# Kernel tuning notes

Hardware: AMD Instinct MI355X
Metric: run time of the kernel (lower is better)

## Reference

```python
import jax, jax.numpy as jnp
import numpy as np

N_NODES = 60000
N_EDGES = 120000
N_GRAPHS = 2048
ATOM_DIM = 4
H = 192            # hidden_dim
NL = 5             # n_layers
ND = 200           # n_descriptors
EDGE_DIM = 1


def setup_inputs() -> dict:
    key = jax.random.key(0)
    ks = jax.random.split(key, 16)

    def w(k, shape, fan_in):
        return jax.random.normal(k, shape, jnp.float32) * (1.0 / np.sqrt(fan_in))

    M_IN = 2 * H + EDGE_DIM  # message MLP input: [x_src, x_dst, edge_attr]
    M_H = 2 * H              # MPNNLayer(hidden_dim=hidden_dim*2)
    inp = {
        "atom_features": jax.random.normal(ks[0], (N_NODES, ATOM_DIM), jnp.float32),
        "edge_attr": jax.random.normal(ks[1], (N_EDGES, EDGE_DIM), jnp.float32),
        "edge_index": jax.random.randint(ks[2], (2, N_EDGES), 0, N_NODES),
        "batch": jnp.sort(jax.random.randint(ks[3], (N_NODES,), 0, N_GRAPHS)),
        # atom encoder: Linear + GELU + LayerNorm
        "enc_w": w(ks[4], (ATOM_DIM, H), ATOM_DIM), "enc_b": jnp.zeros((H,), jnp.float32),
        "enc_ln_g": jnp.ones((H,), jnp.float32), "enc_ln_b": jnp.zeros((H,), jnp.float32),
        # 5 MPNN layers (stacked params)
        "msg_w1": w(ks[5], (NL, M_IN, M_H), M_IN), "msg_b1": jnp.zeros((NL, M_H), jnp.float32),
        "msg_w2": w(ks[6], (NL, M_H, H), M_H), "msg_b2": jnp.zeros((NL, H), jnp.float32),
        "upd_w": w(ks[7], (NL, 2 * H, H), 2 * H), "upd_b": jnp.zeros((NL, H), jnp.float32),
        "ln_g": jnp.ones((NL, H), jnp.float32), "ln_b": jnp.zeros((NL, H), jnp.float32),
        # head MLP: 2H -> H -> H//2 -> ND
        "h1_w": w(ks[8], (2 * H, H), 2 * H), "h1_b": jnp.zeros((H,), jnp.float32),
        "h2_w": w(ks[9], (H, H // 2), H), "h2_b": jnp.zeros((H // 2,), jnp.float32),
        "h3_w": w(ks[10], (H // 2, ND), H // 2), "h3_b": jnp.zeros((ND,), jnp.float32),
    }
    return inp


def _ln(x, g, b, eps=1e-5):
    mu = x.mean(-1, keepdims=True)
    v = x.var(-1, keepdims=True)
    return (x - mu) / jnp.sqrt(v + eps) * g + b


def _gelu(x):
    return jax.nn.gelu(x, approximate=False)  # torch nn.GELU (erf)


def _forward(atom_features, edge_attr, enc_w, enc_b, enc_ln_g, enc_ln_b,
             msg_w1, msg_b1, msg_w2, msg_b2, upd_w, upd_b, ln_g, ln_b,
             h1_w, h1_b, h2_w, h2_b, h3_w, h3_b, edge_index, batch):
    src, dst = edge_index[0], edge_index[1]
    x = _ln(_gelu(atom_features @ enc_w + enc_b), enc_ln_g, enc_ln_b)  # [N, H]
    for l in range(NL):
        # gather endpoints -> message MLP -> scatter-sum to dst
        m_in = jnp.concatenate([x[src], x[dst], edge_attr], axis=-1)   # [E, 2H+1]
        m = _gelu(m_in @ msg_w1[l] + msg_b1[l]) @ msg_w2[l] + msg_b2[l]  # [E, H]
        agg = jax.ops.segment_sum(m, dst, num_segments=N_NODES)        # [N, H]
        x_new = _gelu(jnp.concatenate([x, agg], axis=-1) @ upd_w[l] + upd_b[l])
        x = _ln(x + x_new, ln_g[l], ln_b[l])  # residual + LN (dropout = eval identity)
    # per-graph mean/max pooling (segment reductions)
    cnt = jax.ops.segment_sum(jnp.ones((x.shape[0],), x.dtype), batch, num_segments=N_GRAPHS)
    s = jax.ops.segment_sum(x, batch, num_segments=N_GRAPHS)
    mean_pool = jnp.where(cnt[:, None] > 0, s / jnp.maximum(cnt, 1.0)[:, None], 0.0)
    max_pool = jax.ops.segment_max(x, batch, num_segments=N_GRAPHS)  # -inf for empty, as torch
    g = jnp.concatenate([mean_pool, max_pool], axis=-1)  # [G, 2H]
    h = _gelu(g @ h1_w + h1_b)
    h = _gelu(h @ h2_w + h2_b)
    return h @ h3_w + h3_b  # [G, ND]


def reference(atom_features, edge_attr, edge_index, batch, enc_w, enc_b, enc_ln_g, enc_ln_b,
              msg_w1, msg_b1, msg_w2, msg_b2, upd_w, upd_b, ln_g, ln_b,
              h1_w, h1_b, h2_w, h2_b, h3_w, h3_b):
    return _forward(atom_features, edge_attr, enc_w, enc_b, enc_ln_g, enc_ln_b,
                    msg_w1, msg_b1, msg_w2, msg_b2, upd_w, upd_b, ln_g, ln_b,
                    h1_w, h1_b, h2_w, h2_b, h3_w, h3_b, edge_index, batch)
```

## Files before the change

kernel.cpp:

```cpp
#include <hip/hip_runtime.h>

#define H 192
#define NL 5
#define NN 60000
#define NE 120000
#define NG 2048
#define ND 200
#define LDA 392
#define NT 128
#define LDU 200

typedef __bf16 bfrag __attribute__((ext_vector_type(8)));
typedef __bf16 bf16x4 __attribute__((ext_vector_type(4)));
typedef float f32x4 __attribute__((ext_vector_type(4)));

__device__ __forceinline__ unsigned short f2bf(float f) {
  union { float f; unsigned u; } v; v.f = f;
  return (unsigned short)((v.u + 0x7FFFu + ((v.u >> 16) & 1u)) >> 16);
}
__device__ __forceinline__ float bflo(unsigned u) {
  union { unsigned u; float f; } v; v.u = u << 16; return v.f;
}
__device__ __forceinline__ float bfhi(unsigned u) {
  union { unsigned u; float f; } v; v.u = u & 0xffff0000u; return v.f;
}
__device__ __forceinline__ float gelu(float x) {
  const float t = exp2f(x * (-2.3020922f - 0.10293942f * x * x));
  return x * __frcp_rn(1.f + t);
}

__global__ __launch_bounds__(256) void prep_kernel(
    const float* __restrict__ msg_w1, const float* __restrict__ msg_w2,
    const float* __restrict__ upd_w, const float* __restrict__ h1_w,
    const float* __restrict__ h2_w, const float* __restrict__ h3_w,
    unsigned short* __restrict__ W1f, float* __restrict__ w1last,
    unsigned short* __restrict__ W2f, unsigned short* __restrict__ Uf,
    float* __restrict__ h1t, float* __restrict__ h2t, float* __restrict__ h3t) {
  int idx = blockIdx.x * 256 + threadIdx.x;
  const int SW1 = NL * 147456;
  const int S2 = NL * 384;
  const int SW2 = NL * 73728;
  if (idx < SW1) {
    int l = idx / 147456, r = idx % 147456;
    int i = r & 7, lane = (r >> 3) & 63, t = r >> 9;
    int kk = t % 12, jblk = t / 12;
    int j = jblk * 16 + (lane & 15);
    int k = kk * 32 + ((lane >> 4) << 3) + i;
    W1f[idx] = f2bf(msg_w1[(size_t)l * 385 * 384 + (size_t)k * 384 + j]);
    return;
  }
  idx -= SW1;
  if (idx < S2) {
    int l = idx / 384, j = idx % 384;
    w1last[idx] = msg_w1[(size_t)l * 385 * 384 + 384 * 384 + j];
    return;
  }
  idx -= S2;
  if (idx < SW2) {
    int l = idx / 73728, r = idx % 73728;
    int i = r & 7, lane = (r >> 3) & 63, t = r >> 9;
    int kk = t % 12, jblk = t / 12;
    int j = jblk * 16 + (lane & 15);
    int k = kk * 32 + ((lane >> 4) << 3) + i;
    W2f[idx] = f2bf(msg_w2[(size_t)l * 384 * 192 + (size_t)k * 192 + j]);
    return;
  }
  idx -= SW2;
  if (idx < SW2) {
    int l = idx / 73728, r = idx % 73728;
    int i = r & 7, lane = (r >> 3) & 63, t = r >> 9;
    int kk = t % 12, jblk = t / 12;
    int j = jblk * 16 + (lane & 15);
    int k = kk * 32 + ((lane >> 4) << 3) + i;
    Uf[idx] = f2bf(upd_w[(size_t)l * 384 * 192 + (size_t)k * 192 + j]);
    return;
  }
  idx -= SW2;
  if (idx < 192 * 384) { int j = idx / 384, k = idx % 384; h1t[idx] = h1_w[k * 192 + j]; return; }
  idx -= 192 * 384;
  if (idx < 96 * 192) { int j = idx / 192, k = idx % 192; h2t[idx] = h2_w[k * 96 + j]; return; }
  idx -= 96 * 192;
  if (idx < 200 * 96) { int j = idx / 96, k = idx % 96; h3t[idx] = h3_w[k * 200 + j]; return; }
}

__global__ __launch_bounds__(256) void enc_kernel(
    const float* __restrict__ af, const float* __restrict__ w,
    const float* __restrict__ b, const float* __restrict__ g,
    const float* __restrict__ bb, float* __restrict__ x,
    __bf16* __restrict__ xb) {
  const int node = blockIdx.x * 4 + (threadIdx.x >> 6);
  const int lane = threadIdx.x & 63;
  if (node >= NN) return;
  const float a0 = af[node * 4 + 0], a1 = af[node * 4 + 1];
  const float a2 = af[node * 4 + 2], a3 = af[node * 4 + 3];
  float v[3], s = 0.f, ss = 0.f;
#pragma unroll
  for (int i = 0; i < 3; ++i) {
    const int j = lane + i * 64;
    float o = a0 * w[j] + a1 * w[H + j] + a2 * w[2 * H + j] + a3 * w[3 * H + j] + b[j];
    o = gelu(o);
    v[i] = o; s += o; ss += o * o;
  }
#pragma unroll
  for (int m = 1; m < 64; m <<= 1) { s += __shfl_xor(s, m); ss += __shfl_xor(ss, m); }
  const float mu = s * (1.f / H);
  float var = ss * (1.f / H) - mu * mu;
  const float rstd = rsqrtf(fmaxf(var, 0.f) + 1e-5f);
#pragma unroll
  for (int i = 0; i < 3; ++i) {
    const int j = lane + i * 64;
    const float o = (v[i] - mu) * rstd * g[j] + bb[j];
    x[(size_t)node * H + j] = o;
    xb[(size_t)node * H + j] = (__bf16)o;
  }
}

__global__ __launch_bounds__(256) void csr_count(const int* __restrict__ ei,
                                                 int* __restrict__ deg) {
  const int e = blockIdx.x * 256 + threadIdx.x;
  if (e < NE) atomicAdd(&deg[ei[NE + e]], 1);
}

__global__ __launch_bounds__(1024) void csr_scan(const int* __restrict__ deg,
                                                 int* __restrict__ start) {
  __shared__ int wsum[16];
  const int tid = threadIdx.x, lane = tid & 63, wv = tid >> 6;
  int carry = 0;
  for (int base = 0; base < NN; base += 1024) {
    const int i = base + tid;
    int v = (i < NN) ? deg[i] : 0;
    int s = v;
#pragma unroll
    for (int d = 1; d < 64; d <<= 1) {
      int t = __shfl_up(s, d);
      if (lane >= d) s += t;
    }
    if (lane == 63) wsum[wv] = s;
    __syncthreads();
    if (wv == 0) {
      int ws_ = (lane < 16) ? wsum[lane] : 0;
#pragma unroll
      for (int d = 1; d < 16; d <<= 1) {
        int t = __shfl_up(ws_, d);
        if (lane >= d) ws_ += t;
      }
      if (lane < 16) wsum[lane] = ws_;
    }
    __syncthreads();
    const int woff = (wv == 0) ? 0 : wsum[wv - 1];
    if (i < NN) start[i] = carry + woff + s - v;
    carry += wsum[15];
    __syncthreads();
  }
  if (tid == 0) start[NN] = NE;
}

__global__ __launch_bounds__(256) void csr_fill(const int* __restrict__ ei,
                                                const int* __restrict__ start,
                                                int* __restrict__ cur,
                                                int* __restrict__ eidx) {
  const int e = blockIdx.x * 256 + threadIdx.x;
  if (e < NE) {
    const int d = ei[NE + e];
    const int p = start[d] + atomicAdd(&cur[d], 1);
    eidx[p] = e;
  }
}

__global__ __launch_bounds__(256) void gseg_kernel(const int* __restrict__ batch,
                                                   int* __restrict__ gstart,
                                                   int* __restrict__ gend) {
  const int i = blockIdx.x * 256 + threadIdx.x;
  if (i >= NN) return;
  const int b = batch[i];
  if (i == 0 || batch[i - 1] != b) gstart[b] = i;
  if (i == NN - 1 || batch[i + 1] != b) gend[b] = i + 1;
}

__global__ __launch_bounds__(512, 4) void msg_kernel(
    const __bf16* __restrict__ xb, const int* __restrict__ ei,
    const float* __restrict__ ea, const unsigned short* __restrict__ W1f,
    const float* __restrict__ w1last, const float* __restrict__ b1,
    const unsigned short* __restrict__ W2f, const float* __restrict__ b2,
    unsigned short* __restrict__ m) {
  __shared__ unsigned short A[64 * LDA];
  __shared__ float eaS[64];
  const int tid = threadIdx.x;
  const int wave = tid >> 6, lane = tid & 63;
  const int lrow = lane & 15, kgrp = lane >> 4;
  const int tile = blockIdx.x * 64;

  if (tid < 64) eaS[tid] = ea[tile + tid];
  {
    const int r = tid >> 3, s = tid & 7;
    const int e = tile + r;
    const uint4* ps = (const uint4*)(xb + (size_t)ei[e] * H);
    const uint4* pd = (const uint4*)(xb + (size_t)ei[NE + e] * H);
#pragma unroll
    for (int i = 0; i < 3; ++i)
      *(uint4*)(&A[r * LDA + (s + 8 * i) * 8]) = ps[s + 8 * i];
#pragma unroll
    for (int i = 3; i < 6; ++i)
      *(uint4*)(&A[r * LDA + (s + 8 * i) * 8]) = pd[s + 8 * i - 24];
  }
  __syncthreads();

  const int jb16 = wave * 3;
  f32x4 acc[3][4];
#pragma unroll
  for (int mf = 0; mf < 3; ++mf)
#pragma unroll
    for (int eb = 0; eb < 4; ++eb)
#pragma unroll
      for (int q = 0; q < 4; ++q) acc[mf][eb][q] = 0.f;

#pragma unroll 2
  for (int kk = 0; kk < 12; ++kk) {
    const int k0 = kk * 32 + kgrp * 8;
    bfrag bF[4];
#pragma unroll
    for (int eb = 0; eb < 4; ++eb)
      bF[eb] = *(const bfrag*)(&A[(eb * 16 + lrow) * LDA + k0]);
#pragma unroll
    for (int mf = 0; mf < 3; ++mf) {
      const bfrag aF = *(const bfrag*)(W1f + ((size_t)((jb16 + mf) * 12 + kk) * 64 + lane) * 8);
#pragma unroll
      for (int eb = 0; eb < 4; ++eb)
        acc[mf][eb] = __builtin_amdgcn_mfma_f32_16x16x32_bf16(aF, bF[eb], acc[mf][eb], 0, 0, 0);
    }
  }
  __syncthreads();

#pragma unroll
  for (int mf = 0; mf < 3; ++mf) {
    const int j0 = (jb16 + mf) * 16 + kgrp * 4;
    const float bi0 = b1[j0], bi1 = b1[j0 + 1], bi2 = b1[j0 + 2], bi3 = b1[j0 + 3];
    const float wl0 = w1last[j0], wl1 = w1last[j0 + 1], wl2 = w1last[j0 + 2], wl3 = w1last[j0 + 3];
#pragma unroll
    for (int eb = 0; eb < 4; ++eb) {
      const int e = eb * 16 + lrow;
      const float eav = eaS[e];
      bf16x4 v;
      v[0] = (__bf16)gelu(acc[mf][eb][0] + bi0 + eav * wl0);
      v[1] = (__bf16)gelu(acc[mf][eb][1] + bi1 + eav * wl1);
      v[2] = (__bf16)gelu(acc[mf][eb][2] + bi2 + eav * wl2);
      v[3] = (__bf16)gelu(acc[mf][eb][3] + bi3 + eav * wl3);
      *(bf16x4*)(&A[e * LDA + j0]) = v;
    }
  }
  __syncthreads();

  const int jcnt2 = (wave < 4) ? 2 : 1;
  const int j2b0 = (wave < 4) ? (wave * 2) : (4 + wave);
  f32x4 acc2[2][4];
#pragma unroll
  for (int a = 0; a < 2; ++a)
#pragma unroll
    for (int eb = 0; eb < 4; ++eb)
#pragma unroll
      for (int q = 0; q < 4; ++q) acc2[a][eb][q] = 0.f;

#pragma unroll 2
  for (int kk = 0; kk < 12; ++kk) {
    const int k0 = kk * 32 + kgrp * 8;
    bfrag bF[4];
#pragma unroll
    for (int eb = 0; eb < 4; ++eb)
      bF[eb] = *(const bfrag*)(&A[(eb * 16 + lrow) * LDA + k0]);
#pragma unroll
    for (int a = 0; a < 2; ++a) {
      if (a < jcnt2) {
        const bfrag aF = *(const bfrag*)(W2f + ((size_t)((j2b0 + a) * 12 + kk) * 64 + lane) * 8);
#pragma unroll
        for (int eb = 0; eb < 4; ++eb)
          acc2[a][eb] = __builtin_amdgcn_mfma_f32_16x16x32_bf16(aF, bF[eb], acc2[a][eb], 0, 0, 0);
      }
    }
  }
#pragma unroll
  for (int a = 0; a < 2; ++a) {
    if (a < jcnt2) {
      const int j0 = (j2b0 + a) * 16 + kgrp * 4;
      const float bi0 = b2[j0], bi1 = b2[j0 + 1], bi2 = b2[j0 + 2], bi3 = b2[j0 + 3];
#pragma unroll
      for (int eb = 0; eb < 4; ++eb) {
        const int e = eb * 16 + lrow;
        bf16x4 v;
        v[0] = (__bf16)(acc2[a][eb][0] + bi0);
        v[1] = (__bf16)(acc2[a][eb][1] + bi1);
        v[2] = (__bf16)(acc2[a][eb][2] + bi2);
        v[3] = (__bf16)(acc2[a][eb][3] + bi3);
        *(bf16x4*)(m + (size_t)(tile + e) * H + j0) = v;
      }
    }
  }
}

__global__ __launch_bounds__(512, 4) void upd_kernel(
    const unsigned short* __restrict__ Uf, const float* __restrict__ ub,
    const float* __restrict__ lng, const float* __restrict__ lnb,
    const unsigned short* __restrict__ m, const int* __restrict__ start,
    const int* __restrict__ eidx, float* x, __bf16* xb) {
  __shared__ unsigned short A[NT * LDU];
  __shared__ float wsm[8][NT];
  __shared__ float wsq[8][NT];
  __shared__ float mur[NT], rsr[NT];
  const int tid = threadIdx.x;
  const int wave = tid >> 6, lane = tid & 63;
  const int lrow = lane & 15, kgrp = lane >> 4;
  const int tile = blockIdx.x * NT;

  const int r = tid >> 2, q4 = tid & 3;
  const int node = tile + r;
  if (node < NN) {
    const uint4* px = (const uint4*)(xb + (size_t)node * H + q4 * 48);
#pragma unroll
    for (int i = 0; i < 6; ++i)
      *(uint4*)(&A[r * LDU + q4 * 48 + i * 8]) = px[i];
  } else {
#pragma unroll
    for (int i = 0; i < 6; ++i)
      *(uint4*)(&A[r * LDU + q4 * 48 + i * 8]) = make_uint4(0, 0, 0, 0);
  }
  __syncthreads();

  const int jcnt = (wave < 4) ? 2 : 1;
  const int jb0 = (wave < 4) ? (wave * 2) : (4 + wave);

  f32x4 acc[2][8];
#pragma unroll
  for (int a = 0; a < 2; ++a)
#pragma unroll
    for (int eb = 0; eb < 8; ++eb)
#pragma unroll
      for (int q = 0; q < 4; ++q) acc[a][eb][q] = 0.f;

#pragma unroll 1
  for (int kk = 0; kk < 6; ++kk) {
    const int k0 = kk * 32 + kgrp * 8;
    bfrag bF[8];
#pragma unroll
    for (int eb = 0; eb < 8; ++eb)
      bF[eb] = *(const bfrag*)(&A[(eb * 16 + lrow) * LDU + k0]);
#pragma unroll
    for (int a = 0; a < 2; ++a) {
      if (a < jcnt) {
        const bfrag aF = *(const bfrag*)(Uf + ((size_t)((jb0 + a) * 12 + kk) * 64 + lane) * 8);
#pragma unroll
        for (int eb = 0; eb < 8; ++eb)
          acc[a][eb] = __builtin_amdgcn_mfma_f32_16x16x32_bf16(aF, bF[eb], acc[a][eb], 0, 0, 0);
      }
    }
  }
  __syncthreads();

  if (node < NN) {
    const int p0 = start[node], p1 = start[node + 1];
#pragma unroll
    for (int hh = 0; hh < 2; ++hh) {
      const int c0 = q4 * 48 + hh * 24;
      float av[24];
#pragma unroll
      for (int i = 0; i < 24; ++i) av[i] = 0.f;
      for (int p = p0; p < p1; ++p) {
        const int e = eidx[p];
        const uint4* mr = (const uint4*)(m + (size_t)e * H + c0);
#pragma unroll
        for (int i = 0; i < 3; ++i) {
          const uint4 u = mr[i];
          av[i * 8 + 0] += bflo(u.x); av[i * 8 + 1] += bfhi(u.x);
          av[i * 8 + 2] += bflo(u.y); av[i * 8 + 3] += bfhi(u.y);
          av[i * 8 + 4] += bflo(u.z); av[i * 8 + 5] += bfhi(u.z);
          av[i * 8 + 6] += bflo(u.w); av[i * 8 + 7] += bfhi(u.w);
        }
      }
#pragma unroll
      for (int i = 0; i < 24; i += 4) {
        bf16x4 v;
        v[0] = (__bf16)av[i]; v[1] = (__bf16)av[i + 1];
        v[2] = (__bf16)av[i + 2]; v[3] = (__bf16)av[i + 3];
        *(bf16x4*)(&A[r * LDU + c0 + i]) = v;
      }
    }
  } else {
#pragma unroll
    for (int i = 0; i < 48; i += 8)
      *(uint4*)(&A[r * LDU + q4 * 48 + i]) = make_uint4(0, 0, 0, 0);
  }
  __syncthreads();

#pragma unroll 1
  for (int kk = 0; kk < 6; ++kk) {
    const int k0 = kk * 32 + kgrp * 8;
    bfrag bF[8];
#pragma unroll
    for (int eb = 0; eb < 8; ++eb)
      bF[eb] = *(const bfrag*)(&A[(eb * 16 + lrow) * LDU + k0]);
#pragma unroll
    for (int a = 0; a < 2; ++a) {
      if (a < jcnt) {
        const bfrag aF = *(const bfrag*)(Uf + ((size_t)((jb0 + a) * 12 + 6 + kk) * 64 + lane) * 8);
#pragma unroll
        for (int eb = 0; eb < 8; ++eb)
          acc[a][eb] = __builtin_amdgcn_mfma_f32_16x16x32_bf16(aF, bF[eb], acc[a][eb], 0, 0, 0);
      }
    }
  }

  float lsum[8], lsq[8];
#pragma unroll
  for (int eb = 0; eb < 8; ++eb) { lsum[eb] = 0.f; lsq[eb] = 0.f; }
#pragma unroll
  for (int a = 0; a < 2; ++a) {
    if (a < jcnt) {
      const int jb = (jb0 + a) * 16 + kgrp * 4;
      const float4 ub4 = *(const float4*)(ub + jb);
#pragma unroll
      for (int eb = 0; eb < 8; ++eb) {
        const int n2 = tile + eb * 16 + lrow;
        if (n2 < NN) {
          const float4 xr = *(const float4*)(x + (size_t)n2 * H + jb);
          acc[a][eb][0] = xr.x + gelu(acc[a][eb][0] + ub4.x);
          acc[a][eb][1] = xr.y + gelu(acc[a][eb][1] + ub4.y);
          acc[a][eb][2] = xr.z + gelu(acc[a][eb][2] + ub4.z);
          acc[a][eb][3] = xr.w + gelu(acc[a][eb][3] + ub4.w);
        } else {
          acc[a][eb][0] = 0.f; acc[a][eb][1] = 0.f;
          acc[a][eb][2] = 0.f; acc[a][eb][3] = 0.f;
        }
#pragma unroll
        for (int q = 0; q < 4; ++q) {
          lsum[eb] += acc[a][eb][q];
          lsq[eb] += acc[a][eb][q] * acc[a][eb][q];
        }
      }
    }
  }
#pragma unroll
  for (int eb = 0; eb < 8; ++eb) {
    lsum[eb] += __shfl_xor(lsum[eb], 16);
    lsum[eb] += __shfl_xor(lsum[eb], 32);
    lsq[eb] += __shfl_xor(lsq[eb], 16);
    lsq[eb] += __shfl_xor(lsq[eb], 32);
  }
  if (kgrp == 0) {
#pragma unroll
    for (int eb = 0; eb < 8; ++eb) {
      wsm[wave][eb * 16 + lrow] = lsum[eb];
      wsq[wave][eb * 16 + lrow] = lsq[eb];
    }
  }
  __syncthreads();
  if (tid < NT) {
    float s = 0.f, sq = 0.f;
#pragma unroll
    for (int w2 = 0; w2 < 8; ++w2) { s += wsm[w2][tid]; sq += wsq[w2][tid]; }
    const float mu = s * (1.f / H);
    float var = sq * (1.f / H) - mu * mu;
    mur[tid] = mu;
    rsr[tid] = rsqrtf(fmaxf(var, 0.f) + 1e-5f);
  }
  __syncthreads();
#pragma unroll
  for (int a = 0; a < 2; ++a) {
    if (a < jcnt) {
      const int jb = (jb0 + a) * 16 + kgrp * 4;
      const float4 g4 = *(const float4*)(lng + jb);
      const float4 b4 = *(const float4*)(lnb + jb);
#pragma unroll
      for (int eb = 0; eb < 8; ++eb) {
        const int nc = eb * 16 + lrow;
        const int n2 = tile + nc;
        if (n2 < NN) {
          const float mu = mur[nc], rs = rsr[nc];
          float4 o;
          o.x = (acc[a][eb][0] - mu) * rs * g4.x + b4.x;
          o.y = (acc[a][eb][1] - mu) * rs * g4.y + b4.y;
          o.z = (acc[a][eb][2] - mu) * rs * g4.z + b4.z;
          o.w = (acc[a][eb][3] - mu) * rs * g4.w + b4.w;
          *(float4*)(x + (size_t)n2 * H + jb) = o;
          bf16x4 ob;
          ob[0] = (__bf16)o.x; ob[1] = (__bf16)o.y;
          ob[2] = (__bf16)o.z; ob[3] = (__bf16)o.w;
          *(bf16x4*)(xb + (size_t)n2 * H + jb) = ob;
        }
      }
    }
  }
}

__global__ __launch_bounds__(256) void head_kernel(
    const float* __restrict__ x, const int* __restrict__ gstart,
    const int* __restrict__ gend,
    const float* __restrict__ h1t, const float* __restrict__ h1b,
    const float* __restrict__ h2t, const float* __restrict__ h2b,
    const float* __restrict__ h3t, const float* __restrict__ h3b,
    float* __restrict__ out) {
  __shared__ float G[4][2 * H];
  __shared__ float Hs[4][H];
  __shared__ float H2s[4][96];
  const int w = threadIdx.x >> 6, lane = threadIdx.x & 63;
  const int gi = blockIdx.x * 4 + w;
  const int n0 = gstart[gi], n1 = gend[gi];
  float sm[3] = {0.f, 0.f, 0.f};
  float mx[3] = {-INFINITY, -INFINITY, -INFINITY};
  for (int n = n0; n < n1; ++n) {
#pragma unroll
    for (int i = 0; i < 3; ++i) {
      const float v = x[(size_t)n * H + lane + i * 64];
      sm[i] += v; mx[i] = fmaxf(mx[i], v);
    }
  }
  const int cnt = n1 - n0;
  const float inv = cnt > 0 ? 1.f / (float)cnt : 0.f;
#pragma unroll
  for (int i = 0; i < 3; ++i) {
    const int j = lane + i * 64;
    G[w][j] = sm[i] * inv;
    G[w][H + j] = mx[i];
  }
  __syncthreads();
#pragma unroll
  for (int i = 0; i < 3; ++i) {
    const int j = lane + i * 64;
    const float4* wr4 = (const float4*)(h1t + (size_t)j * 384);
    float s = h1b[j];
    for (int k4 = 0; k4 < 96; ++k4) {
      float4 ww = wr4[k4];
      s += G[w][k4 * 4 + 0] * ww.x + G[w][k4 * 4 + 1] * ww.y +
           G[w][k4 * 4 + 2] * ww.z + G[w][k4 * 4 + 3] * ww.w;
    }
    Hs[w][j] = gelu(s);
  }
  __syncthreads();
  for (int j = lane; j < 96; j += 64) {
    const float4* wr4 = (const float4*)(h2t + (size_t)j * 192);
    float s = h2b[j];
    for (int k4 = 0; k4 < 48; ++k4) {
      float4 ww = wr4[k4];
      s += Hs[w][k4 * 4 + 0] * ww.x + Hs[w][k4 * 4 + 1] * ww.y +
           Hs[w][k4 * 4 + 2] * ww.z + Hs[w][k4 * 4 + 3] * ww.w;
    }
    H2s[w][j] = gelu(s);
  }
  __syncthreads();
  for (int j = lane; j < 200; j += 64) {
    const float4* wr4 = (const float4*)(h3t + (size_t)j * 96);
    float s = h3b[j];
    for (int k4 = 0; k4 < 24; ++k4) {
      float4 ww = wr4[k4];
      s += H2s[w][k4 * 4 + 0] * ww.x + H2s[w][k4 * 4 + 1] * ww.y +
           H2s[w][k4 * 4 + 2] * ww.z + H2s[w][k4 * 4 + 3] * ww.w;
    }
    out[(size_t)gi * ND + j] = s;
  }
}

extern "C" void kernel_launch(void* const* d_in, const int* in_sizes, int n_in,
                              void* d_out, int out_size, void* d_ws, size_t ws_size,
                              hipStream_t stream) {
  const float* atom   = (const float*)d_in[0];
  const float* ea     = (const float*)d_in[1];
  const int*   ei     = (const int*)d_in[2];
  const int*   batch  = (const int*)d_in[3];
  const float* enc_w  = (const float*)d_in[4];
  const float* enc_b  = (const float*)d_in[5];
  const float* enc_lng= (const float*)d_in[6];
  const float* enc_lnb= (const float*)d_in[7];
  const float* msg_w1 = (const float*)d_in[8];
  const float* msg_b1 = (const float*)d_in[9];
  const float* msg_w2 = (const float*)d_in[10];
  const float* msg_b2 = (const float*)d_in[11];
  const float* upd_w  = (const float*)d_in[12];
  const float* upd_b  = (const float*)d_in[13];
  const float* ln_g   = (const float*)d_in[14];
  const float* ln_b   = (const float*)d_in[15];
  const float* h1_w   = (const float*)d_in[16];
  const float* h1_b   = (const float*)d_in[17];
  const float* h2_w   = (const float*)d_in[18];
  const float* h2_b   = (const float*)d_in[19];
  const float* h3_w   = (const float*)d_in[20];
  const float* h3_b   = (const float*)d_in[21];
  float* out = (float*)d_out;

  char* ws = (char*)d_ws;
  size_t off = 0;
  auto alloc = [&](size_t bytes) -> void* {
    void* p = ws + off;
    off = (off + bytes + 255) & ~(size_t)255;
    return p;
  };
  float* x            = (float*)alloc((size_t)NN * H * 4);
  __bf16* xb          = (__bf16*)alloc((size_t)NN * H * 2);
  unsigned short* msg = (unsigned short*)alloc((size_t)NE * H * 2);
  unsigned short* W1f = (unsigned short*)alloc((size_t)NL * 147456 * 2);
  float* w1last       = (float*)alloc((size_t)NL * 384 * 4);
  unsigned short* W2f = (unsigned short*)alloc((size_t)NL * 73728 * 2);
  unsigned short* Uf  = (unsigned short*)alloc((size_t)NL * 73728 * 2);
  float* h1t          = (float*)alloc((size_t)192 * 384 * 4);
  float* h2t          = (float*)alloc((size_t)96 * 192 * 4);
  float* h3t          = (float*)alloc((size_t)200 * 96 * 4);
  int* deg            = (int*)alloc((size_t)NN * 4);
  int* cstart         = (int*)alloc((size_t)(NN + 1) * 4);
  int* eidx           = (int*)alloc((size_t)NE * 4);
  int* gstart         = (int*)alloc((size_t)NG * 4);
  int* gend           = (int*)alloc((size_t)NG * 4);

  prep_kernel<<<6203, 256, 0, stream>>>(msg_w1, msg_w2, upd_w, h1_w, h2_w, h3_w,
                                        W1f, w1last, W2f, Uf, h1t, h2t, h3t);
  enc_kernel<<<NN / 4, 256, 0, stream>>>(atom, enc_w, enc_b, enc_lng, enc_lnb, x, xb);

  hipMemsetAsync(deg, 0, (size_t)NN * 4, stream);
  csr_count<<<(NE + 255) / 256, 256, 0, stream>>>(ei, deg);
  csr_scan<<<1, 1024, 0, stream>>>(deg, cstart);
  hipMemsetAsync(deg, 0, (size_t)NN * 4, stream);
  csr_fill<<<(NE + 255) / 256, 256, 0, stream>>>(ei, cstart, deg, eidx);

  hipMemsetAsync(gstart, 0, (size_t)NG * 4, stream);
  hipMemsetAsync(gend, 0, (size_t)NG * 4, stream);
  gseg_kernel<<<(NN + 255) / 256, 256, 0, stream>>>(batch, gstart, gend);

  for (int l = 0; l < NL; ++l) {
    msg_kernel<<<NE / 64, 512, 0, stream>>>(
        xb, ei, ea, W1f + (size_t)l * 147456, w1last + l * 384,
        msg_b1 + l * 384, W2f + (size_t)l * 73728, msg_b2 + l * 192, msg);
    upd_kernel<<<(NN + NT - 1) / NT, 512, 0, stream>>>(
        Uf + (size_t)l * 73728, upd_b + l * 192, ln_g + l * 192,
        ln_b + l * 192, msg, cstart, eidx, x, xb);
  }
  head_kernel<<<NG / 4, 256, 0, stream>>>(x, gstart, gend, h1t, h1_b, h2t, h2_b,
                                          h3t, h3_b, out);
}
```

Before: 929.2 us.

## Split pooling from head MLP and run head on bf16 MFMA tiles

Pooling now writes bf16 graph features to a buffer, and a separate head kernel runs the three-layer MLP with bf16 MFMA on 32-graph tiles using pre-swizzled bf16 weights. Before, each wave did scalar fp32 dot products per graph and re-read the weights from global memory. This adds one kernel launch and a global round trip for the pooled features, and lowers head precision to bf16.

```diff
diff --git a/kernel.cpp b/kernel.cpp
--- a/kernel.cpp
+++ b/kernel.cpp
@@ -35,7 +35,8 @@
     const float* __restrict__ h2_w, const float* __restrict__ h3_w,
     unsigned short* __restrict__ W1f, float* __restrict__ w1last,
     unsigned short* __restrict__ W2f, unsigned short* __restrict__ Uf,
-    float* __restrict__ h1t, float* __restrict__ h2t, float* __restrict__ h3t) {
+    unsigned short* __restrict__ h1f, unsigned short* __restrict__ h2f,
+    unsigned short* __restrict__ h3f) {
   int idx = blockIdx.x * 256 + threadIdx.x;
   const int SW1 = NL * 147456;
   const int S2 = NL * 384;
@@ -76,11 +77,32 @@
     return;
   }
   idx -= SW2;
-  if (idx < 192 * 384) { int j = idx / 384, k = idx % 384; h1t[idx] = h1_w[k * 192 + j]; return; }
-  idx -= 192 * 384;
-  if (idx < 96 * 192) { int j = idx / 192, k = idx % 192; h2t[idx] = h2_w[k * 96 + j]; return; }
-  idx -= 96 * 192;
-  if (idx < 200 * 96) { int j = idx / 96, k = idx % 96; h3t[idx] = h3_w[k * 200 + j]; return; }
+  if (idx < 73728) {
+    int i = idx & 7, lane = (idx >> 3) & 63, t = idx >> 9;
+    int kk = t % 12, jblk = t / 12;
+    int j = jblk * 16 + (lane & 15);
+    int k = kk * 32 + ((lane >> 4) << 3) + i;
+    h1f[idx] = f2bf(h1_w[(size_t)k * 192 + j]);
+    return;
+  }
+  idx -= 73728;
+  if (idx < 18432) {
+    int i = idx & 7, lane = (idx >> 3) & 63, t = idx >> 9;
+    int kk = t % 6, jblk = t / 6;
+    int j = jblk * 16 + (lane & 15);
+    int k = kk * 32 + ((lane >> 4) << 3) + i;
+    h2f[idx] = f2bf(h2_w[(size_t)k * 96 + j]);
+    return;
+  }
+  idx -= 18432;
+  if (idx < 19968) {
+    int i = idx & 7, lane = (idx >> 3) & 63, t = idx >> 9;
+    int kk = t % 3, jblk = t / 3;
+    int j = jblk * 16 + (lane & 15);
+    int k = kk * 32 + ((lane >> 4) << 3) + i;
+    h3f[idx] = (j < 200) ? f2bf(h3_w[(size_t)k * 200 + j]) : (unsigned short)0;
+    return;
+  }
 }
 
 __global__ __launch_bounds__(256) void enc_kernel(
@@ -489,16 +511,9 @@
   }
 }
 
-__global__ __launch_bounds__(256) void head_kernel(
+__global__ __launch_bounds__(256) void pool_kernel(
     const float* __restrict__ x, const int* __restrict__ gstart,
-    const int* __restrict__ gend,
-    const float* __restrict__ h1t, const float* __restrict__ h1b,
-    const float* __restrict__ h2t, const float* __restrict__ h2b,
-    const float* __restrict__ h3t, const float* __restrict__ h3b,
-    float* __restrict__ out) {
-  __shared__ float G[4][2 * H];
-  __shared__ float Hs[4][H];
-  __shared__ float H2s[4][96];
+    const int* __restrict__ gend, __bf16* __restrict__ Gb) {
   const int w = threadIdx.x >> 6, lane = threadIdx.x & 63;
   const int gi = blockIdx.x * 4 + w;
   const int n0 = gstart[gi], n1 = gend[gi];
@@ -516,43 +531,162 @@
 #pragma unroll
   for (int i = 0; i < 3; ++i) {
     const int j = lane + i * 64;
-    G[w][j] = sm[i] * inv;
-    G[w][H + j] = mx[i];
-  }
-  __syncthreads();
-#pragma unroll
-  for (int i = 0; i < 3; ++i) {
-    const int j = lane + i * 64;
-    const float4* wr4 = (const float4*)(h1t + (size_t)j * 384);
-    float s = h1b[j];
-    for (int k4 = 0; k4 < 96; ++k4) {
-      float4 ww = wr4[k4];
-      s += G[w][k4 * 4 + 0] * ww.x + G[w][k4 * 4 + 1] * ww.y +
-           G[w][k4 * 4 + 2] * ww.z + G[w][k4 * 4 + 3] * ww.w;
-    }
-    Hs[w][j] = gelu(s);
-  }
-  __syncthreads();
-  for (int j = lane; j < 96; j += 64) {
-    const float4* wr4 = (const float4*)(h2t + (size_t)j * 192);
-    float s = h2b[j];
-    for (int k4 = 0; k4 < 48; ++k4) {
-      float4 ww = wr4[k4];
-      s += Hs[w][k4 * 4 + 0] * ww.x + Hs[w][k4 * 4 + 1] * ww.y +
-           Hs[w][k4 * 4 + 2] * ww.z + Hs[w][k4 * 4 + 3] * ww.w;
-    }
-    H2s[w][j] = gelu(s);
-  }
-  __syncthreads();
-  for (int j = lane; j < 200; j += 64) {
-    const float4* wr4 = (const float4*)(h3t + (size_t)j * 96);
-    float s = h3b[j];
-    for (int k4 = 0; k4 < 24; ++k4) {
-      float4 ww = wr4[k4];
-      s += H2s[w][k4 * 4 + 0] * ww.x + H2s[w][k4 * 4 + 1] * ww.y +
-           H2s[w][k4 * 4 + 2] * ww.z + H2s[w][k4 * 4 + 3] * ww.w;
-    }
-    out[(size_t)gi * ND + j] = s;
+    Gb[(size_t)gi * 384 + j] = (__bf16)(sm[i] * inv);
+    Gb[(size_t)gi * 384 + 192 + j] = (__bf16)mx[i];
+  }
+}
+
+__global__ __launch_bounds__(512) void head_kernel(
+    const __bf16* __restrict__ Gb,
+    const unsigned short* __restrict__ h1f, const float* __restrict__ h1b,
+    const unsigned short* __restrict__ h2f, const float* __restrict__ h2b,
+    const unsigned short* __restrict__ h3f, const float* __restrict__ h3b,
+    float* __restrict__ out) {
+  __shared__ unsigned short A[32 * LDA];
+  const int tid = threadIdx.x;
+  const int wave = tid >> 6, lane = tid & 63;
+  const int lrow = lane & 15, kgrp = lane >> 4;
+  const int tile = blockIdx.x * 32;
+
+  {
+    const int r = tid >> 4, s = tid & 15;
+    const uint4* pg = (const uint4*)(Gb + (size_t)(tile + r) * 384);
+#pragma unroll
+    for (int i = 0; i < 3; ++i)
+      *(uint4*)(&A[r * LDA + (s + 16 * i) * 8]) = pg[s + 16 * i];
+  }
+  __syncthreads();
+
+  const int jcnt1 = (wave < 4) ? 2 : 1;
+  const int jb1 = (wave < 4) ? (wave * 2) : (4 + wave);
+  f32x4 acc[2][2];
+#pragma unroll
+  for (int a = 0; a < 2; ++a)
+#pragma unroll
+    for (int eb = 0; eb < 2; ++eb)
+#pragma unroll
+      for (int q = 0; q < 4; ++q) acc[a][eb][q] = 0.f;
+#pragma unroll 2
+  for (int kk = 0; kk < 12; ++kk) {
+    const int k0 = kk * 32 + kgrp * 8;
+    bfrag bF[2];
+#pragma unroll
+    for (int eb = 0; eb < 2; ++eb)
+      bF[eb] = *(const bfrag*)(&A[(eb * 16 + lrow) * LDA + k0]);
+#pragma unroll
+    for (int a = 0; a < 2; ++a) {
+      if (a < jcnt1) {
+        const bfrag aF = *(const bfrag*)(h1f + ((size_t)((jb1 + a) * 12 + kk) * 64 + lane) * 8);
+#pragma unroll
+        for (int eb = 0; eb < 2; ++eb)
+          acc[a][eb] = __builtin_amdgcn_mfma_f32_16x16x32_bf16(aF, bF[eb], acc[a][eb], 0, 0, 0);
+      }
+    }
+  }
+  __syncthreads();
+#pragma unroll
+  for (int a = 0; a < 2; ++a) {
+    if (a < jcnt1) {
+      const int j0 = (jb1 + a) * 16 + kgrp * 4;
+      const float4 b4 = *(const float4*)(h1b + j0);
+#pragma unroll
+      for (int eb = 0; eb < 2; ++eb) {
+        const int g = eb * 16 + lrow;
+        bf16x4 v;
+        v[0] = (__bf16)gelu(acc[a][eb][0] + b4.x);
+        v[1] = (__bf16)gelu(acc[a][eb][1] + b4.y);
+        v[2] = (__bf16)gelu(acc[a][eb][2] + b4.z);
+        v[3] = (__bf16)gelu(acc[a][eb][3] + b4.w);
+        *(bf16x4*)(&A[g * LDA + j0]) = v;
+      }
+    }
+  }
+  __syncthreads();
+
+  f32x4 acc2[2];
+#pragma unroll
+  for (int eb = 0; eb < 2; ++eb)
+#pragma unroll
+    for (int q = 0; q < 4; ++q) acc2[eb][q] = 0.f;
+  if (wave < 6) {
+#pragma unroll 2
+    for (int kk = 0; kk < 6; ++kk) {
+      const int k0 = kk * 32 + kgrp * 8;
+      bfrag bF[2];
+#pragma unroll
+      for (int eb = 0; eb < 2; ++eb)
+        bF[eb] = *(const bfrag*)(&A[(eb * 16 + lrow) * LDA + k0]);
+      const bfrag aF = *(const bfrag*)(h2f + ((size_t)(wave * 6 + kk) * 64 + lane) * 8);
+#pragma unroll
+      for (int eb = 0; eb < 2; ++eb)
+        acc2[eb] = __builtin_amdgcn_mfma_f32_16x16x32_bf16(aF, bF[eb], acc2[eb], 0, 0, 0);
+    }
+    const int j0 = wave * 16 + kgrp * 4;
+    const float4 b4 = *(const float4*)(h2b + j0);
+#pragma unroll
+    for (int eb = 0; eb < 2; ++eb) {
+      const int g = eb * 16 + lrow;
+      bf16x4 v;
+      v[0] = (__bf16)gelu(acc2[eb][0] + b4.x);
+      v[1] = (__bf16)gelu(acc2[eb][1] + b4.y);
+      v[2] = (__bf16)gelu(acc2[eb][2] + b4.z);
+      v[3] = (__bf16)gelu(acc2[eb][3] + b4.w);
+      *(bf16x4*)(&A[g * LDA + 192 + j0]) = v;
+    }
+  }
+  __syncthreads();
+
+  const int jcnt3 = (wave < 5) ? 2 : 1;
+  const int jb3 = (wave < 5) ? (wave * 2) : (wave + 5);
+  f32x4 acc3[2][2];
+#pragma unroll
+  for (int a = 0; a < 2; ++a)
+#pragma unroll
+    for (int eb = 0; eb < 2; ++eb)
+#pragma unroll
+      for (int q = 0; q < 4; ++q) acc3[a][eb][q] = 0.f;
+#pragma unroll
+  for (int kk = 0; kk < 3; ++kk) {
+    const int k0 = 192 + kk * 32 + kgrp * 8;
+    bfrag bF[2];
+#pragma unroll
+    for (int eb = 0; eb < 2; ++eb)
+      bF[eb] = *(const bfrag*)(&A[(eb * 16 + lrow) * LDA + k0]);
+#pragma unroll
+    for (int a = 0; a < 2; ++a) {
+      if (a < jcnt3) {
+        const bfrag aF = *(const bfrag*)(h3f + ((size_t)((jb3 + a) * 3 + kk) * 64 + lane) * 8);
+#pragma unroll
+        for (int eb = 0; eb < 2; ++eb)
+          acc3[a][eb] = __builtin_amdgcn_mfma_f32_16x16x32_bf16(aF, bF[eb], acc3[a][eb], 0, 0, 0);
+      }
+    }
+  }
+#pragma unroll
+  for (int a = 0; a < 2; ++a) {
+    if (a < jcnt3) {
+      const int jb = jb3 + a;
+      const int j0 = jb * 16 + kgrp * 4;
+#pragma unroll
+      for (int eb = 0; eb < 2; ++eb) {
+        const int g = tile + eb * 16 + lrow;
+        if (jb < 12) {
+          const float4 b4 = *(const float4*)(h3b + j0);
+          float4 o;
+          o.x = acc3[a][eb][0] + b4.x;
+          o.y = acc3[a][eb][1] + b4.y;
+          o.z = acc3[a][eb][2] + b4.z;
+          o.w = acc3[a][eb][3] + b4.w;
+          *(float4*)(out + (size_t)g * ND + j0) = o;
+        } else {
+#pragma unroll
+          for (int t = 0; t < 4; ++t) {
+            const int j = j0 + t;
+            if (j < ND) out[(size_t)g * ND + j] = acc3[a][eb][t] + h3b[j];
+          }
+        }
+      }
+    }
   }
 }
 
@@ -597,17 +731,18 @@
   float* w1last       = (float*)alloc((size_t)NL * 384 * 4);
   unsigned short* W2f = (unsigned short*)alloc((size_t)NL * 73728 * 2);
   unsigned short* Uf  = (unsigned short*)alloc((size_t)NL * 73728 * 2);
-  float* h1t          = (float*)alloc((size_t)192 * 384 * 4);
-  float* h2t          = (float*)alloc((size_t)96 * 192 * 4);
-  float* h3t          = (float*)alloc((size_t)200 * 96 * 4);
+  unsigned short* h1f = (unsigned short*)alloc((size_t)73728 * 2);
+  unsigned short* h2f = (unsigned short*)alloc((size_t)18432 * 2);
+  unsigned short* h3f = (unsigned short*)alloc((size_t)19968 * 2);
+  __bf16* Gb          = (__bf16*)alloc((size_t)NG * 384 * 2);
   int* deg            = (int*)alloc((size_t)NN * 4);
   int* cstart         = (int*)alloc((size_t)(NN + 1) * 4);
   int* eidx           = (int*)alloc((size_t)NE * 4);
   int* gstart         = (int*)alloc((size_t)NG * 4);
   int* gend           = (int*)alloc((size_t)NG * 4);
 
-  prep_kernel<<<6203, 256, 0, stream>>>(msg_w1, msg_w2, upd_w, h1_w, h2_w, h3_w,
-                                        W1f, w1last, W2f, Uf, h1t, h2t, h3t);
+  prep_kernel<<<6206, 256, 0, stream>>>(msg_w1, msg_w2, upd_w, h1_w, h2_w, h3_w,
+                                        W1f, w1last, W2f, Uf, h1f, h2f, h3f);
   enc_kernel<<<NN / 4, 256, 0, stream>>>(atom, enc_w, enc_b, enc_lng, enc_lnb, x, xb);
 
   hipMemsetAsync(deg, 0, (size_t)NN * 4, stream);
@@ -628,6 +763,6 @@
         Uf + (size_t)l * 73728, upd_b + l * 192, ln_g + l * 192,
         ln_b + l * 192, msg, cstart, eidx, x, xb);
   }
-  head_kernel<<<NG / 4, 256, 0, stream>>>(x, gstart, gend, h1t, h1_b, h2t, h2_b,
-                                          h3t, h3_b, out);
-}
+  pool_kernel<<<NG / 4, 256, 0, stream>>>(x, gstart, gend, Gb);
+  head_kernel<<<NG / 32, 512, 0, stream>>>(Gb, h1f, h1_b, h2f, h2_b, h3f, h3_b, out);
+}
```

Measured after the change: 853.6 us. 8.1% less time.
